# Kernel optimization log

Measured on AMD Instinct MI355X. Metric: run time of the kernel, lower is better.

The kernel has to match this reference:

```python
import jax, jax.numpy as jnp
import numpy as np

N_NODES = 100000
N_EDGES = 1600000
D = 128


def _gine_layer(x, src, dst, e, W1, b1, W2, b2):
    # message: relu(x_j + e_ji), aggregate: sum at destination
    m = jax.nn.relu(x[src] + e)                       # [E, D]
    agg = jax.ops.segment_sum(m, dst, num_segments=x.shape[0])  # [N, D]
    h = agg + x                                       # (1 + eps) * x_i with eps = 0
    h = jax.nn.relu(jnp.dot(h, W1) + b1)
    return jnp.dot(h, W2) + b2


def setup_inputs() -> dict:
    key = jax.random.key(0)
    ks = jax.random.split(key, 16)
    s = 0.05
    inp = {
        "x": jax.random.normal(ks[0], (N_NODES, D), dtype=jnp.float32),
        "edge_index": jax.random.randint(ks[1], (2, N_EDGES), 0, N_NODES, dtype=jnp.int64) if jax.config.jax_enable_x64 else jax.random.randint(ks[1], (2, N_EDGES), 0, N_NODES, dtype=jnp.int32),
        "edge_attr": jax.random.randint(ks[2], (N_EDGES,), 0, 100, dtype=jnp.int32),
        "edge_emb": jax.random.normal(ks[3], (100, D), dtype=jnp.float32) * s,
        "Win": jax.random.normal(ks[4], (D, D), dtype=jnp.float32) * s,
        "b_in": jnp.zeros((D,), dtype=jnp.float32),
        "W1_0": jax.random.normal(ks[5], (D, D), dtype=jnp.float32) * s,
        "b1_0": jnp.zeros((D,), dtype=jnp.float32),
        "W2_0": jax.random.normal(ks[6], (D, D), dtype=jnp.float32) * s,
        "b2_0": jnp.zeros((D,), dtype=jnp.float32),
        "W1_1": jax.random.normal(ks[7], (D, D), dtype=jnp.float32) * s,
        "b1_1": jnp.zeros((D,), dtype=jnp.float32),
        "W2_1": jax.random.normal(ks[8], (D, D), dtype=jnp.float32) * s,
        "b2_1": jnp.zeros((D,), dtype=jnp.float32),
        "Wout": jax.random.normal(ks[9], (D, 1), dtype=jnp.float32) * s,
        "b_out": jnp.zeros((1,), dtype=jnp.float32),
    }
    return inp


def reference(x, edge_index, edge_attr, edge_emb, Win, b_in,
              W1_0, b1_0, W2_0, b2_0, W1_1, b1_1, W2_1, b2_1,
              Wout, b_out):
    src, dst = edge_index[0], edge_index[1]
    e = edge_emb[edge_attr]                 # [E, D] edge-attribute embedding lookup
    h = jnp.dot(x, Win) + b_in              # input_proj
    # layer 0: GINEConv + residual add + relu (norm=none, dropout off)
    h = jax.nn.relu(_gine_layer(h, src, dst, e, W1_0, b1_0, W2_0, b2_0) + h)
    # layer 1
    h = jax.nn.relu(_gine_layer(h, src, dst, e, W1_1, b1_1, W2_1, b2_1) + h)
    # output_mlp: single Linear(hidden, 1); no final activation, no pooling
    return jnp.dot(h, Wout) + b_out
```

## Files before the change

kernel.cpp:

```cpp
#include <hip/hip_runtime.h>

#define NN 100000
#define D 128
#define CHUNK 4096
#define BCSTRIDE 392
#define AGG_BLOCKS 1024

typedef __attribute__((ext_vector_type(8))) short short8;
typedef __attribute__((ext_vector_type(8))) unsigned short ushort8;
typedef __attribute__((ext_vector_type(4))) float f32x4;

__device__ __forceinline__ float4 ld4(const float* p) { return *(const float4*)p; }

__device__ __forceinline__ unsigned short f2bf(float f) {
    unsigned int u = __float_as_uint(f);
    unsigned int r = u + 0x7fffu + ((u >> 16) & 1u);
    return (unsigned short)(r >> 16);
}
__device__ __forceinline__ float bf2f(unsigned short h) {
    return __uint_as_float(((unsigned int)h) << 16);
}
__device__ __forceinline__ int swz(int r, int c) {
    return r * 128 + ((((c >> 2) ^ (r & 7)) << 2) | (c & 3));
}

__device__ __forceinline__ void coop_gemm(
    const unsigned int* uT,
    const unsigned short* __restrict__ Whi, const unsigned short* __restrict__ Wlo,
    int wv, int L, int lr, int q, f32x4 acc[4][2])
{
    #pragma unroll
    for (int ks = 0; ks < 4; ++ks) {
        short8 ahi[4], alo[4];
        #pragma unroll
        for (int m = 0; m < 4; ++m) {
            const int row = m * 16 + lr;
            const int cb  = ks * 32 + q * 8;
            const uint4 a0 = *(const uint4*)&uT[swz(row, cb)];
            const uint4 a1 = *(const uint4*)&uT[swz(row, cb + 4)];
            const unsigned int w[8] = {a0.x, a0.y, a0.z, a0.w, a1.x, a1.y, a1.z, a1.w};
            #pragma unroll
            for (int j = 0; j < 8; ++j) {
                ahi[m][j] = (short)(w[j] >> 16);
                alo[m][j] = (short)(w[j] & 0xffffu);
            }
        }
        #pragma unroll
        for (int n = 0; n < 2; ++n) {
            const int nt = wv * 2 + n;
            const int base = ((nt * 4 + ks) * 64 + L) * 8;
            const short8 bhi = *(const short8*)&Whi[base];
            const short8 blo = *(const short8*)&Wlo[base];
            #pragma unroll
            for (int m = 0; m < 4; ++m) {
                acc[m][n] = __builtin_amdgcn_mfma_f32_16x16x32_bf16(alo[m], bhi, acc[m][n], 0, 0, 0);
                acc[m][n] = __builtin_amdgcn_mfma_f32_16x16x32_bf16(ahi[m], blo, acc[m][n], 0, 0, 0);
                acc[m][n] = __builtin_amdgcn_mfma_f32_16x16x32_bf16(ahi[m], bhi, acc[m][n], 0, 0, 0);
            }
        }
    }
}

__device__ __forceinline__ void gemm_in_body(
    unsigned int* uT, int bid,
    const float* __restrict__ A1,
    const unsigned short* __restrict__ Whi, const unsigned short* __restrict__ Wlo,
    const float* __restrict__ bias,
    unsigned short* __restrict__ out_hi, unsigned short* __restrict__ out_lo, int N)
{
    const int t  = threadIdx.x;
    const int wv = t >> 6;
    const int L  = t & 63;
    const int lr = L & 15;
    const int q  = L >> 4;
    const int rbase = wv * 16;
    const int row = bid * 64 + rbase + lr;
    const int rl  = rbase + lr;

    #pragma unroll
    for (int ks = 0; ks < 4; ++ks) {
        float v[8];
        if (row < N) {
            const int off = row * D + ks * 32 + q * 8;
            const float4 x0 = ld4(&A1[off]), x1 = ld4(&A1[off + 4]);
            v[0] = x0.x; v[1] = x0.y; v[2] = x0.z; v[3] = x0.w;
            v[4] = x1.x; v[5] = x1.y; v[6] = x1.z; v[7] = x1.w;
        } else {
            #pragma unroll
            for (int j = 0; j < 8; ++j) v[j] = 0.f;
        }
        unsigned int pk[8];
        #pragma unroll
        for (int j = 0; j < 8; ++j) {
            const unsigned int hi = f2bf(v[j]);
            pk[j] = (hi << 16) | f2bf(v[j] - bf2f((unsigned short)hi));
        }
        const int cb = ks * 32 + q * 8;
        *(uint4*)&uT[swz(rl, cb)]     = make_uint4(pk[0], pk[1], pk[2], pk[3]);
        *(uint4*)&uT[swz(rl, cb + 4)] = make_uint4(pk[4], pk[5], pk[6], pk[7]);
    }
    __syncthreads();

    f32x4 acc[4][2];
    #pragma unroll
    for (int m = 0; m < 4; ++m)
        #pragma unroll
        for (int n = 0; n < 2; ++n) acc[m][n] = (f32x4){0.f, 0.f, 0.f, 0.f};
    coop_gemm(uT, Whi, Wlo, wv, L, lr, q, acc);
    __syncthreads();

    #pragma unroll
    for (int n = 0; n < 2; ++n) {
        const int nt = wv * 2 + n;
        const float b = bias[nt * 16 + lr];
        #pragma unroll
        for (int m = 0; m < 4; ++m)
            #pragma unroll
            for (int r = 0; r < 4; ++r)
                uT[swz(m * 16 + q * 4 + r, nt * 16 + lr)] = __float_as_uint(acc[m][n][r] + b);
    }
    __syncthreads();

    if (row < N) {
        #pragma unroll
        for (int ks = 0; ks < 4; ++ks) {
            const int cb = ks * 32 + q * 8;
            const uint4 a0 = *(const uint4*)&uT[swz(rl, cb)];
            const uint4 a1 = *(const uint4*)&uT[swz(rl, cb + 4)];
            const unsigned int w[8] = {a0.x, a0.y, a0.z, a0.w, a1.x, a1.y, a1.z, a1.w};
            const int off = row * D + cb;
            ushort8 oh, ol;
            #pragma unroll
            for (int j = 0; j < 8; ++j) {
                const float o = __uint_as_float(w[j]);
                const unsigned short h = f2bf(o);
                oh[j] = h;
                ol[j] = f2bf(o - bf2f(h));
            }
            *(ushort8*)&out_hi[off] = oh;
            *(ushort8*)&out_lo[off] = ol;
        }
    }
}

__global__ __launch_bounds__(256) void setup_all(
    const float* __restrict__ W0, const float* __restrict__ W1,
    const float* __restrict__ W2, const float* __restrict__ W3,
    const float* __restrict__ W4, unsigned short* __restrict__ wp,
    const float* __restrict__ emb, unsigned int* __restrict__ embp,
    int* __restrict__ binTotal)
{
    const int T = blockIdx.x * 256 + threadIdx.x;
    if (T < 5 * D * D) {
        const int w = T / (D * D);
        const int t = T % (D * D);
        const float* W = (w == 0) ? W0 : (w == 1) ? W1 : (w == 2) ? W2 : (w == 3) ? W3 : W4;
        const int j  = t & 7;
        const int L  = (t >> 3) & 63;
        const int ks = (t >> 9) & 3;
        const int nt = t >> 11;
        const float v = W[(ks * 32 + (L >> 4) * 8 + j) * D + nt * 16 + (L & 15)];
        const unsigned short h = f2bf(v);
        unsigned short* hi = wp + (size_t)w * 2 * D * D;
        hi[t] = h;
        hi[D * D + t] = f2bf(v - bf2f(h));
    } else if (T < 5 * D * D + 6400) {
        const int i = T - 5 * D * D;
        embp[i] = (unsigned int)f2bf(emb[i * 2]) | ((unsigned int)f2bf(emb[i * 2 + 1]) << 16);
    } else if (T < 5 * D * D + 6400 + BCSTRIDE) {
        binTotal[T - 5 * D * D - 6400] = 0;
    }
}

__global__ __launch_bounds__(256) void fuse_count_gemm(
    const int* __restrict__ dst, int* __restrict__ blkcnt,
    int* __restrict__ binTotal, int E, int nbins, int csrB,
    const float* __restrict__ A1,
    const unsigned short* __restrict__ Whi, const unsigned short* __restrict__ Wlo,
    const float* __restrict__ bias,
    unsigned short* __restrict__ out_hi, unsigned short* __restrict__ out_lo,
    int N, int gemmBase)
{
    __shared__ __align__(16) unsigned int uT[64 * 128];
    if ((int)blockIdx.x < csrB) {
        int* hist = (int*)uT;
        const int t = threadIdx.x;
        const int i = blockIdx.x;
        for (int k = t; k < nbins; k += 256) hist[k] = 0;
        __syncthreads();
        const int e0 = i * CHUNK;
        const int e1 = min(E, e0 + CHUNK);
        for (int e = e0 + t; e < e1; e += 256) atomicAdd(&hist[dst[e] >> 8], 1);
        __syncthreads();
        for (int k = t; k < nbins; k += 256) {
            const int c = hist[k];
            blkcnt[i * BCSTRIDE + k] = c;
            if (c) atomicAdd(&binTotal[k], c);
        }
    } else {
        gemm_in_body(uT, blockIdx.x - csrB + gemmBase, A1, Whi, Wlo, bias, out_hi, out_lo, N);
    }
}

__global__ __launch_bounds__(512) void bin_scan(
    const int* __restrict__ binTotal, int* __restrict__ binStart,
    int* __restrict__ binCursor, int nbins)
{
    __shared__ int s[512];
    const int t = threadIdx.x;
    const int v = (t < nbins) ? binTotal[t] : 0;
    s[t] = v;
    __syncthreads();
    for (int off = 1; off < 512; off <<= 1) {
        const int x = (t >= off) ? s[t - off] : 0;
        __syncthreads();
        s[t] += x;
        __syncthreads();
    }
    if (t < nbins) { binStart[t] = s[t] - v; binCursor[t] = s[t] - v; }
    if (t == 0)    binStart[nbins] = s[511];
}

__global__ __launch_bounds__(256) void fuse_scatter_gemm(
    const int* __restrict__ src, const int* __restrict__ dst,
    const int* __restrict__ attr, const int* __restrict__ blkcnt,
    int* __restrict__ binCursor, int2* __restrict__ binned, int E, int nbins, int csrB,
    const float* __restrict__ A1,
    const unsigned short* __restrict__ Whi, const unsigned short* __restrict__ Wlo,
    const float* __restrict__ bias,
    unsigned short* __restrict__ out_hi, unsigned short* __restrict__ out_lo,
    int N, int gemmBase)
{
    __shared__ __align__(16) unsigned int uT[64 * 128];
    if ((int)blockIdx.x < csrB) {
        int* cur = (int*)uT;
        const int t = threadIdx.x;
        const int i = blockIdx.x;
        for (int k = t; k < nbins; k += 256) {
            const int c = blkcnt[i * BCSTRIDE + k];
            if (c) cur[k] = atomicAdd(&binCursor[k], c);
        }
        __syncthreads();
        const int e0 = i * CHUNK;
        const int e1 = min(E, e0 + CHUNK);
        for (int e = e0 + t; e < e1; e += 256) {
            const int d = dst[e];
            const int p = atomicAdd(&cur[d >> 8], 1);
            binned[p] = make_int2(src[e] | (attr[e] << 20), d);
        }
    } else {
        gemm_in_body(uT, blockIdx.x - csrB + gemmBase, A1, Whi, Wlo, bias, out_hi, out_lo, N);
    }
}

__global__ __launch_bounds__(256) void fuse_build_gemm(
    const int2* __restrict__ binned, const int* __restrict__ binStart,
    int* __restrict__ rowptr, int* __restrict__ epack, int csrB,
    const float* __restrict__ A1,
    const unsigned short* __restrict__ Whi, const unsigned short* __restrict__ Wlo,
    const float* __restrict__ bias,
    unsigned short* __restrict__ out_hi, unsigned short* __restrict__ out_lo,
    int N, int gemmBase)
{
    __shared__ __align__(16) unsigned int uT[64 * 128];
    if ((int)blockIdx.x < csrB) {
        int* hist = (int*)uT;
        int* scn  = (int*)uT + 256;
        int* curn = (int*)uT + 512;
        const int t = threadIdx.x;
        const int b = blockIdx.x;
        hist[t] = 0;
        __syncthreads();
        const int ebeg = binStart[b];
        const int eend = binStart[b + 1];
        for (int e = ebeg + t; e < eend; e += 256) atomicAdd(&hist[binned[e].y & 255], 1);
        __syncthreads();
        scn[t] = hist[t];
        __syncthreads();
        for (int off = 1; off < 256; off <<= 1) {
            const int x = (t >= off) ? scn[t - off] : 0;
            __syncthreads();
            scn[t] += x;
            __syncthreads();
        }
        const int node = b * 256 + t;
        if (node < N) rowptr[node] = ebeg + scn[t];
        curn[t] = ebeg + scn[t] - hist[t];
        __syncthreads();
        for (int e = ebeg + t; e < eend; e += 256) {
            const int2 v = binned[e];
            const int p = atomicAdd(&curn[v.y & 255], 1);
            epack[p] = v.x;
        }
    } else {
        gemm_in_body(uT, blockIdx.x - csrB + gemmBase, A1, Whi, Wlo, bias, out_hi, out_lo, N);
    }
}

template<bool LAST>
__global__ __launch_bounds__(256) void mlp_fused(
    const float* __restrict__ agg,
    const unsigned short* h_hi, const unsigned short* h_lo,
    const unsigned short* __restrict__ W1hi, const unsigned short* __restrict__ W1lo,
    const float* __restrict__ b1,
    const unsigned short* __restrict__ W2hi, const unsigned short* __restrict__ W2lo,
    const float* __restrict__ b2,
    unsigned short* out_hi, unsigned short* out_lo,
    const float* __restrict__ Wout, const float* __restrict__ bout,
    float* __restrict__ outv, int N)
{
    __shared__ __align__(16) unsigned int uT[64 * 128];
    const int t  = threadIdx.x;
    const int wv = t >> 6;
    const int L  = t & 63;
    const int lr = L & 15;
    const int q  = L >> 4;
    const int rbase = wv * 16;
    const int row = blockIdx.x * 64 + rbase + lr;
    const int rl  = rbase + lr;

    #pragma unroll
    for (int ks = 0; ks < 4; ++ks) {
        float v[8];
        if (row < N) {
            const int off = row * D + ks * 32 + q * 8;
            const float4 x0 = ld4(&agg[off]), x1 = ld4(&agg[off + 4]);
            const ushort8 hh = *(const ushort8*)&h_hi[off];
            const ushort8 ll = *(const ushort8*)&h_lo[off];
            v[0] = x0.x; v[1] = x0.y; v[2] = x0.z; v[3] = x0.w;
            v[4] = x1.x; v[5] = x1.y; v[6] = x1.z; v[7] = x1.w;
            #pragma unroll
            for (int j = 0; j < 8; ++j) v[j] += bf2f(hh[j]) + bf2f(ll[j]);
        } else {
            #pragma unroll
            for (int j = 0; j < 8; ++j) v[j] = 0.f;
        }
        unsigned int pk[8];
        #pragma unroll
        for (int j = 0; j < 8; ++j) {
            const unsigned int hi = f2bf(v[j]);
            pk[j] = (hi << 16) | f2bf(v[j] - bf2f((unsigned short)hi));
        }
        const int cb = ks * 32 + q * 8;
        *(uint4*)&uT[swz(rl, cb)]     = make_uint4(pk[0], pk[1], pk[2], pk[3]);
        *(uint4*)&uT[swz(rl, cb + 4)] = make_uint4(pk[4], pk[5], pk[6], pk[7]);
    }
    __syncthreads();

    f32x4 acc[4][2];
    #pragma unroll
    for (int m = 0; m < 4; ++m)
        #pragma unroll
        for (int n = 0; n < 2; ++n) acc[m][n] = (f32x4){0.f, 0.f, 0.f, 0.f};
    coop_gemm(uT, W1hi, W1lo, wv, L, lr, q, acc);
    __syncthreads();

    #pragma unroll
    for (int n = 0; n < 2; ++n) {
        const int nt = wv * 2 + n;
        const float b = b1[nt * 16 + lr];
        #pragma unroll
        for (int m = 0; m < 4; ++m)
            #pragma unroll
            for (int r = 0; r < 4; ++r) {
                const float o = fmaxf(acc[m][n][r] + b, 0.f);
                const unsigned int hi = f2bf(o);
                const unsigned int lo = f2bf(o - bf2f((unsigned short)hi));
                uT[swz(m * 16 + q * 4 + r, nt * 16 + lr)] = (hi << 16) | lo;
            }
    }
    __syncthreads();

    f32x4 acc2[4][2];
    #pragma unroll
    for (int m = 0; m < 4; ++m)
        #pragma unroll
        for (int n = 0; n < 2; ++n) acc2[m][n] = (f32x4){0.f, 0.f, 0.f, 0.f};
    coop_gemm(uT, W2hi, W2lo, wv, L, lr, q, acc2);
    __syncthreads();

    #pragma unroll
    for (int n = 0; n < 2; ++n) {
        const int nt = wv * 2 + n;
        const float b = b2[nt * 16 + lr];
        #pragma unroll
        for (int m = 0; m < 4; ++m)
            #pragma unroll
            for (int r = 0; r < 4; ++r)
                uT[swz(m * 16 + q * 4 + r, nt * 16 + lr)] = __float_as_uint(acc2[m][n][r] + b);
    }
    __syncthreads();

    if (LAST) {
        float accv = 0.f;
        if (row < N) {
            #pragma unroll
            for (int ks = 0; ks < 4; ++ks) {
                const int cb = ks * 32 + q * 8;
                const uint4 a0 = *(const uint4*)&uT[swz(rl, cb)];
                const uint4 a1 = *(const uint4*)&uT[swz(rl, cb + 4)];
                const unsigned int w[8] = {a0.x, a0.y, a0.z, a0.w, a1.x, a1.y, a1.z, a1.w};
                const int off = row * D + cb;
                const ushort8 hh = *(const ushort8*)&h_hi[off];
                const ushort8 ll = *(const ushort8*)&h_lo[off];
                const float4 w0 = ld4(&Wout[cb]);
                const float4 w1 = ld4(&Wout[cb + 4]);
                float o[8];
                #pragma unroll
                for (int j = 0; j < 8; ++j)
                    o[j] = fmaxf(__uint_as_float(w[j]) + bf2f(hh[j]) + bf2f(ll[j]), 0.f);
                accv += o[0] * w0.x + o[1] * w0.y + o[2] * w0.z + o[3] * w0.w;
                accv += o[4] * w1.x + o[5] * w1.y + o[6] * w1.z + o[7] * w1.w;
            }
        }
        accv += __shfl_xor(accv, 16);
        accv += __shfl_xor(accv, 32);
        if (q == 0 && row < N) outv[row] = accv + bout[0];
    } else if (row < N) {
        #pragma unroll
        for (int ks = 0; ks < 4; ++ks) {
            const int cb = ks * 32 + q * 8;
            const uint4 a0 = *(const uint4*)&uT[swz(rl, cb)];
            const uint4 a1 = *(const uint4*)&uT[swz(rl, cb + 4)];
            const unsigned int w[8] = {a0.x, a0.y, a0.z, a0.w, a1.x, a1.y, a1.z, a1.w};
            const int off = row * D + cb;
            const ushort8 hh = *(const ushort8*)&h_hi[off];
            const ushort8 ll = *(const ushort8*)&h_lo[off];
            ushort8 oh, ol;
            #pragma unroll
            for (int j = 0; j < 8; ++j) {
                const float o = fmaxf(__uint_as_float(w[j]) + bf2f(hh[j]) + bf2f(ll[j]), 0.f);
                const unsigned short h = f2bf(o);
                oh[j] = h;
                ol[j] = f2bf(o - bf2f(h));
            }
            *(ushort8*)&out_hi[off] = oh;
            *(ushort8*)&out_lo[off] = ol;
        }
    }
}

__global__ __launch_bounds__(512) void aggregate(
    const unsigned int* __restrict__ hu,
    const int* __restrict__ rowptr, const int* __restrict__ epack,
    const unsigned int* __restrict__ embp, float* __restrict__ agg, int N)
{
    __shared__ unsigned int semb[100 * 64];
    const int t = threadIdx.x;
    for (int i = t; i < 100 * 64; i += 512) semb[i] = embp[i];
    __syncthreads();

    const int wv   = t >> 6;
    const int lane = t & 63;

    for (int node = blockIdx.x * 8 + wv; node < N; node += AGG_BLOCKS * 8) {
        int start = (node == 0) ? 0 : rowptr[node - 1];
        int end   = rowptr[node];
        start = __builtin_amdgcn_readfirstlane(start);
        end   = __builtin_amdgcn_readfirstlane(end);

        float ax = 0.f, ay = 0.f;
        int j = start;

        for (; j < end && (j & 3); ++j) {
            const int p0 = __builtin_amdgcn_readfirstlane(epack[j]);
            const unsigned int u0 = hu[(p0 & 0xFFFFF) * 64 + lane];
            const unsigned int v0 = semb[(p0 >> 20) * 64 + lane];
            ax += fmaxf(__uint_as_float(u0 << 16) + __uint_as_float(v0 << 16), 0.f);
            ay += fmaxf(__uint_as_float(u0 & 0xffff0000u) + __uint_as_float(v0 & 0xffff0000u), 0.f);
        }

        for (; j + 7 < end; j += 8) {
            const int4 pk0 = *(const int4*)&epack[j];
            const int4 pk1 = *(const int4*)&epack[j + 4];
            int p[8];
            p[0] = __builtin_amdgcn_readfirstlane(pk0.x);
            p[1] = __builtin_amdgcn_readfirstlane(pk0.y);
            p[2] = __builtin_amdgcn_readfirstlane(pk0.z);
            p[3] = __builtin_amdgcn_readfirstlane(pk0.w);
            p[4] = __builtin_amdgcn_readfirstlane(pk1.x);
            p[5] = __builtin_amdgcn_readfirstlane(pk1.y);
            p[6] = __builtin_amdgcn_readfirstlane(pk1.z);
            p[7] = __builtin_amdgcn_readfirstlane(pk1.w);
            unsigned int u[8], v[8];
            #pragma unroll
            for (int k = 0; k < 8; ++k) u[k] = hu[(p[k] & 0xFFFFF) * 64 + lane];
            #pragma unroll
            for (int k = 0; k < 8; ++k) v[k] = semb[(p[k] >> 20) * 64 + lane];
            #pragma unroll
            for (int k = 0; k < 8; ++k) {
                ax += fmaxf(__uint_as_float(u[k] << 16) + __uint_as_float(v[k] << 16), 0.f);
                ay += fmaxf(__uint_as_float(u[k] & 0xffff0000u) + __uint_as_float(v[k] & 0xffff0000u), 0.f);
            }
        }

        if (j + 3 < end) {
            const int4 pk0 = *(const int4*)&epack[j];
            int p[4];
            p[0] = __builtin_amdgcn_readfirstlane(pk0.x);
            p[1] = __builtin_amdgcn_readfirstlane(pk0.y);
            p[2] = __builtin_amdgcn_readfirstlane(pk0.z);
            p[3] = __builtin_amdgcn_readfirstlane(pk0.w);
            unsigned int u[4], v[4];
            #pragma unroll
            for (int k = 0; k < 4; ++k) u[k] = hu[(p[k] & 0xFFFFF) * 64 + lane];
            #pragma unroll
            for (int k = 0; k < 4; ++k) v[k] = semb[(p[k] >> 20) * 64 + lane];
            #pragma unroll
            for (int k = 0; k < 4; ++k) {
                ax += fmaxf(__uint_as_float(u[k] << 16) + __uint_as_float(v[k] << 16), 0.f);
                ay += fmaxf(__uint_as_float(u[k] & 0xffff0000u) + __uint_as_float(v[k] & 0xffff0000u), 0.f);
            }
            j += 4;
        }

        for (; j < end; ++j) {
            const int p0 = __builtin_amdgcn_readfirstlane(epack[j]);
            const unsigned int u0 = hu[(p0 & 0xFFFFF) * 64 + lane];
            const unsigned int v0 = semb[(p0 >> 20) * 64 + lane];
            ax += fmaxf(__uint_as_float(u0 << 16) + __uint_as_float(v0 << 16), 0.f);
            ay += fmaxf(__uint_as_float(u0 & 0xffff0000u) + __uint_as_float(v0 & 0xffff0000u), 0.f);
        }

        float2 o; o.x = ax; o.y = ay;
        ((float2*)agg)[node * 64 + lane] = o;
    }
}

extern "C" void kernel_launch(void* const* d_in, const int* in_sizes, int n_in,
                              void* d_out, int out_size, void* d_ws, size_t ws_size,
                              hipStream_t stream)
{
    const float* x     = (const float*)d_in[0];
    const int*   ei    = (const int*)  d_in[1];
    const int*   attr  = (const int*)  d_in[2];
    const float* emb   = (const float*)d_in[3];
    const float* Win   = (const float*)d_in[4];
    const float* b_in  = (const float*)d_in[5];
    const float* W1_0  = (const float*)d_in[6];
    const float* b1_0  = (const float*)d_in[7];
    const float* W2_0  = (const float*)d_in[8];
    const float* b2_0  = (const float*)d_in[9];
    const float* W1_1  = (const float*)d_in[10];
    const float* b1_1  = (const float*)d_in[11];
    const float* W2_1  = (const float*)d_in[12];
    const float* b2_1  = (const float*)d_in[13];
    const float* Wout  = (const float*)d_in[14];
    const float* b_out = (const float*)d_in[15];
    float* out = (float*)d_out;

    const int N = NN;
    const int E = in_sizes[2];
    const int* srcp = ei;
    const int* dstp = ei + E;
    const int nbins = (N + 255) >> 8;
    const int eblocks = (E + CHUNK - 1) / CHUNK;

    unsigned short* h_hi = (unsigned short*)d_ws;
    unsigned short* h_lo = h_hi + (size_t)N * D;
    float* agg    = (float*)(h_lo + (size_t)N * D);
    int*   rowptr = (int*)(agg + (size_t)N * D);
    int*   epack  = rowptr + N;
    unsigned short* wp = (unsigned short*)(epack + E);
    unsigned short* Whi[5], *Wlo[5];
    for (int i = 0; i < 5; ++i) {
        Whi[i] = wp + (size_t)i * 2 * D * D;
        Wlo[i] = Whi[i] + D * D;
    }
    unsigned int* embp = (unsigned int*)(wp + 5 * 2 * D * D);
    int2* binned    = (int2*)agg;
    int*  blkcnt    = (int*)(binned + E);
    int*  binTotal  = blkcnt + eblocks * BCSTRIDE;
    int*  binStart  = binTotal + BCSTRIDE;
    int*  binCursor = binStart + BCSTRIDE;

    dim3 blk(256);
    const int fgrid = (N + 63) / 64;
    const int sgrid = (5 * D * D + 6400 + BCSTRIDE + 255) / 256;

    const int G1 = 200;
    const int G2 = 700;
    const int G3 = fgrid - G1 - G2;

    setup_all<<<sgrid, blk, 0, stream>>>(Win, W1_0, W2_0, W1_1, W2_1, wp, emb, embp, binTotal);

    fuse_count_gemm<<<eblocks + G1, blk, 0, stream>>>(
        dstp, blkcnt, binTotal, E, nbins, eblocks,
        x, Whi[0], Wlo[0], b_in, h_hi, h_lo, N, 0);
    bin_scan<<<1, 512, 0, stream>>>(binTotal, binStart, binCursor, nbins);
    fuse_scatter_gemm<<<eblocks + G2, blk, 0, stream>>>(
        srcp, dstp, attr, blkcnt, binCursor, binned, E, nbins, eblocks,
        x, Whi[0], Wlo[0], b_in, h_hi, h_lo, N, G1);
    fuse_build_gemm<<<nbins + G3, blk, 0, stream>>>(
        binned, binStart, rowptr, epack, nbins,
        x, Whi[0], Wlo[0], b_in, h_hi, h_lo, N, G1 + G2);

    aggregate<<<AGG_BLOCKS, dim3(512), 0, stream>>>(
        (const unsigned int*)h_hi, rowptr, epack, embp, agg, N);
    mlp_fused<false><<<fgrid, blk, 0, stream>>>(
        agg, h_hi, h_lo, Whi[1], Wlo[1], b1_0, Whi[2], Wlo[2], b2_0,
        h_hi, h_lo, nullptr, nullptr, nullptr, N);

    aggregate<<<AGG_BLOCKS, dim3(512), 0, stream>>>(
        (const unsigned int*)h_hi, rowptr, epack, embp, agg, N);
    mlp_fused<true><<<fgrid, blk, 0, stream>>>(
        agg, h_hi, h_lo, Whi[3], Wlo[3], b1_1, Whi[4], Wlo[4], b2_1,
        nullptr, nullptr, Wout, b_out, out, N);
}
```

Baseline: 429.6 us.

## Use 8-wave 512-thread blocks for fused GEMM and CSR-build kernels

Doubles the block size of the fused GEMM, CSR count/scatter/build and MLP kernels from 256 to 512 threads. Each wave now owns one 16-column output tile instead of two. The global load/store mapping is reorganised so each lane handles 16 contiguous columns of one row, with the final output reduction done over 8 lanes. The aim is more waves in flight per 64-row tile and fewer B-operand loads per wave, at the cost of more threads contending for the same shared-memory tile and barriers, and larger per-thread register arrays.

```diff
diff --git a/kernel.cpp b/kernel.cpp
--- a/kernel.cpp
+++ b/kernel.cpp
@@ -24,10 +24,10 @@
     return r * 128 + ((((c >> 2) ^ (r & 7)) << 2) | (c & 3));
 }
 
-__device__ __forceinline__ void coop_gemm(
+__device__ __forceinline__ void coop_gemm8(
     const unsigned int* uT,
     const unsigned short* __restrict__ Whi, const unsigned short* __restrict__ Wlo,
-    int wv, int L, int lr, int q, f32x4 acc[4][2])
+    int wv, int lane, int lr, int q, f32x4 acc[4])
 {
     #pragma unroll
     for (int ks = 0; ks < 4; ++ks) {
@@ -45,18 +45,14 @@
                 alo[m][j] = (short)(w[j] & 0xffffu);
             }
         }
-        #pragma unroll
-        for (int n = 0; n < 2; ++n) {
-            const int nt = wv * 2 + n;
-            const int base = ((nt * 4 + ks) * 64 + L) * 8;
-            const short8 bhi = *(const short8*)&Whi[base];
-            const short8 blo = *(const short8*)&Wlo[base];
-            #pragma unroll
-            for (int m = 0; m < 4; ++m) {
-                acc[m][n] = __builtin_amdgcn_mfma_f32_16x16x32_bf16(alo[m], bhi, acc[m][n], 0, 0, 0);
-                acc[m][n] = __builtin_amdgcn_mfma_f32_16x16x32_bf16(ahi[m], blo, acc[m][n], 0, 0, 0);
-                acc[m][n] = __builtin_amdgcn_mfma_f32_16x16x32_bf16(ahi[m], bhi, acc[m][n], 0, 0, 0);
-            }
+        const int base = ((wv * 4 + ks) * 64 + lane) * 8;
+        const short8 bhi = *(const short8*)&Whi[base];
+        const short8 blo = *(const short8*)&Wlo[base];
+        #pragma unroll
+        for (int m = 0; m < 4; ++m) {
+            acc[m] = __builtin_amdgcn_mfma_f32_16x16x32_bf16(alo[m], bhi, acc[m], 0, 0, 0);
+            acc[m] = __builtin_amdgcn_mfma_f32_16x16x32_bf16(ahi[m], blo, acc[m], 0, 0, 0);
+            acc[m] = __builtin_amdgcn_mfma_f32_16x16x32_bf16(ahi[m], bhi, acc[m], 0, 0, 0);
         }
     }
 }
@@ -68,77 +64,78 @@
     const float* __restrict__ bias,
     unsigned short* __restrict__ out_hi, unsigned short* __restrict__ out_lo, int N)
 {
-    const int t  = threadIdx.x;
-    const int wv = t >> 6;
-    const int L  = t & 63;
-    const int lr = L & 15;
-    const int q  = L >> 4;
-    const int rbase = wv * 16;
-    const int row = bid * 64 + rbase + lr;
-    const int rl  = rbase + lr;
-
+    const int t    = threadIdx.x;
+    const int wv   = t >> 6;
+    const int lane = t & 63;
+    const int lr   = lane & 15;
+    const int q    = lane >> 4;
+    const int rE   = wv * 8 + (lane >> 3);
+    const int cE   = (lane & 7) * 16;
+    const int rowE = bid * 64 + rE;
+
+    {
+        float v[16];
+        if (rowE < N) {
+            const int off = rowE * D + cE;
+            #pragma unroll
+            for (int k = 0; k < 4; ++k) {
+                const float4 x = ld4(&A1[off + k * 4]);
+                v[k * 4 + 0] = x.x; v[k * 4 + 1] = x.y; v[k * 4 + 2] = x.z; v[k * 4 + 3] = x.w;
+            }
+        } else {
+            #pragma unroll
+            for (int j = 0; j < 16; ++j) v[j] = 0.f;
+        }
+        #pragma unroll
+        for (int k = 0; k < 4; ++k) {
+            unsigned int pk[4];
+            #pragma unroll
+            for (int j = 0; j < 4; ++j) {
+                const float f = v[k * 4 + j];
+                const unsigned int hi = f2bf(f);
+                pk[j] = (hi << 16) | f2bf(f - bf2f((unsigned short)hi));
+            }
+            *(uint4*)&uT[swz(rE, cE + k * 4)] = make_uint4(pk[0], pk[1], pk[2], pk[3]);
+        }
+    }
+    __syncthreads();
+
+    f32x4 acc[4];
     #pragma unroll
-    for (int ks = 0; ks < 4; ++ks) {
-        float v[8];
-        if (row < N) {
-            const int off = row * D + ks * 32 + q * 8;
-            const float4 x0 = ld4(&A1[off]), x1 = ld4(&A1[off + 4]);
-            v[0] = x0.x; v[1] = x0.y; v[2] = x0.z; v[3] = x0.w;
-            v[4] = x1.x; v[5] = x1.y; v[6] = x1.z; v[7] = x1.w;
-        } else {
-            #pragma unroll
-            for (int j = 0; j < 8; ++j) v[j] = 0.f;
-        }
-        unsigned int pk[8];
-        #pragma unroll
-        for (int j = 0; j < 8; ++j) {
-            const unsigned int hi = f2bf(v[j]);
-            pk[j] = (hi << 16) | f2bf(v[j] - bf2f((unsigned short)hi));
-        }
-        const int cb = ks * 32 + q * 8;
-        *(uint4*)&uT[swz(rl, cb)]     = make_uint4(pk[0], pk[1], pk[2], pk[3]);
-        *(uint4*)&uT[swz(rl, cb + 4)] = make_uint4(pk[4], pk[5], pk[6], pk[7]);
-    }
-    __syncthreads();
-
-    f32x4 acc[4][2];
-    #pragma unroll
-    for (int m = 0; m < 4; ++m)
-        #pragma unroll
-        for (int n = 0; n < 2; ++n) acc[m][n] = (f32x4){0.f, 0.f, 0.f, 0.f};
-    coop_gemm(uT, Whi, Wlo, wv, L, lr, q, acc);
-    __syncthreads();
-
-    #pragma unroll
-    for (int n = 0; n < 2; ++n) {
-        const int nt = wv * 2 + n;
-        const float b = bias[nt * 16 + lr];
+    for (int m = 0; m < 4; ++m) acc[m] = (f32x4){0.f, 0.f, 0.f, 0.f};
+    coop_gemm8(uT, Whi, Wlo, wv, lane, lr, q, acc);
+    __syncthreads();
+
+    {
+        const float b = bias[wv * 16 + lr];
         #pragma unroll
         for (int m = 0; m < 4; ++m)
             #pragma unroll
             for (int r = 0; r < 4; ++r)
-                uT[swz(m * 16 + q * 4 + r, nt * 16 + lr)] = __float_as_uint(acc[m][n][r] + b);
-    }
-    __syncthreads();
-
-    if (row < N) {
-        #pragma unroll
-        for (int ks = 0; ks < 4; ++ks) {
-            const int cb = ks * 32 + q * 8;
-            const uint4 a0 = *(const uint4*)&uT[swz(rl, cb)];
-            const uint4 a1 = *(const uint4*)&uT[swz(rl, cb + 4)];
-            const unsigned int w[8] = {a0.x, a0.y, a0.z, a0.w, a1.x, a1.y, a1.z, a1.w};
-            const int off = row * D + cb;
+                uT[swz(m * 16 + q * 4 + r, wv * 16 + lr)] = __float_as_uint(acc[m][r] + b);
+    }
+    __syncthreads();
+
+    if (rowE < N) {
+        const int off = rowE * D + cE;
+        unsigned int w[16];
+        #pragma unroll
+        for (int k = 0; k < 4; ++k) {
+            const uint4 a = *(const uint4*)&uT[swz(rE, cE + k * 4)];
+            w[k * 4 + 0] = a.x; w[k * 4 + 1] = a.y; w[k * 4 + 2] = a.z; w[k * 4 + 3] = a.w;
+        }
+        #pragma unroll
+        for (int h8 = 0; h8 < 2; ++h8) {
             ushort8 oh, ol;
             #pragma unroll
             for (int j = 0; j < 8; ++j) {
-                const float o = __uint_as_float(w[j]);
+                const float o = __uint_as_float(w[h8 * 8 + j]);
                 const unsigned short h = f2bf(o);
                 oh[j] = h;
                 ol[j] = f2bf(o - bf2f(h));
             }
-            *(ushort8*)&out_hi[off] = oh;
-            *(ushort8*)&out_lo[off] = ol;
+            *(ushort8*)&out_hi[off + h8 * 8] = oh;
+            *(ushort8*)&out_lo[off + h8 * 8] = ol;
         }
     }
 }
@@ -172,7 +169,7 @@
     }
 }
 
-__global__ __launch_bounds__(256) void fuse_count_gemm(
+__global__ __launch_bounds__(512, 8) void fuse_count_gemm(
     const int* __restrict__ dst, int* __restrict__ blkcnt,
     int* __restrict__ binTotal, int E, int nbins, int csrB,
     const float* __restrict__ A1,
@@ -186,13 +183,13 @@
         int* hist = (int*)uT;
         const int t = threadIdx.x;
         const int i = blockIdx.x;
-        for (int k = t; k < nbins; k += 256) hist[k] = 0;
+        for (int k = t; k < nbins; k += 512) hist[k] = 0;
         __syncthreads();
         const int e0 = i * CHUNK;
         const int e1 = min(E, e0 + CHUNK);
-        for (int e = e0 + t; e < e1; e += 256) atomicAdd(&hist[dst[e] >> 8], 1);
-        __syncthreads();
-        for (int k = t; k < nbins; k += 256) {
+        for (int e = e0 + t; e < e1; e += 512) atomicAdd(&hist[dst[e] >> 8], 1);
+        __syncthreads();
+        for (int k = t; k < nbins; k += 512) {
             const int c = hist[k];
             blkcnt[i * BCSTRIDE + k] = c;
             if (c) atomicAdd(&binTotal[k], c);
@@ -221,7 +218,7 @@
     if (t == 0)    binStart[nbins] = s[511];
 }
 
-__global__ __launch_bounds__(256) void fuse_scatter_gemm(
+__global__ __launch_bounds__(512, 8) void fuse_scatter_gemm(
     const int* __restrict__ src, const int* __restrict__ dst,
     const int* __restrict__ attr, const int* __restrict__ blkcnt,
     int* __restrict__ binCursor, int2* __restrict__ binned, int E, int nbins, int csrB,
@@ -236,14 +233,14 @@
         int* cur = (int*)uT;
         const int t = threadIdx.x;
         const int i = blockIdx.x;
-        for (int k = t; k < nbins; k += 256) {
+        for (int k = t; k < nbins; k += 512) {
             const int c = blkcnt[i * BCSTRIDE + k];
             if (c) cur[k] = atomicAdd(&binCursor[k], c);
         }
         __syncthreads();
         const int e0 = i * CHUNK;
         const int e1 = min(E, e0 + CHUNK);
-        for (int e = e0 + t; e < e1; e += 256) {
+        for (int e = e0 + t; e < e1; e += 512) {
             const int d = dst[e];
             const int p = atomicAdd(&cur[d >> 8], 1);
             binned[p] = make_int2(src[e] | (attr[e] << 20), d);
@@ -253,7 +250,7 @@
     }
 }
 
-__global__ __launch_bounds__(256) void fuse_build_gemm(
+__global__ __launch_bounds__(512, 8) void fuse_build_gemm(
     const int2* __restrict__ binned, const int* __restrict__ binStart,
     int* __restrict__ rowptr, int* __restrict__ epack, int csrB,
     const float* __restrict__ A1,
@@ -269,25 +266,28 @@
         int* curn = (int*)uT + 512;
         const int t = threadIdx.x;
         const int b = blockIdx.x;
-        hist[t] = 0;
+        if (t < 256) hist[t] = 0;
         __syncthreads();
         const int ebeg = binStart[b];
         const int eend = binStart[b + 1];
-        for (int e = ebeg + t; e < eend; e += 256) atomicAdd(&hist[binned[e].y & 255], 1);
-        __syncthreads();
-        scn[t] = hist[t];
+        for (int e = ebeg + t; e < eend; e += 512) atomicAdd(&hist[binned[e].y & 255], 1);
+        __syncthreads();
+        if (t < 256) scn[t] = hist[t];
         __syncthreads();
         for (int off = 1; off < 256; off <<= 1) {
-            const int x = (t >= off) ? scn[t - off] : 0;
+            int x = 0;
+            if (t < 256 && t >= off) x = scn[t - off];
             __syncthreads();
-            scn[t] += x;
+            if (t < 256) scn[t] += x;
             __syncthreads();
         }
-        const int node = b * 256 + t;
-        if (node < N) rowptr[node] = ebeg + scn[t];
-        curn[t] = ebeg + scn[t] - hist[t];
-        __syncthreads();
-        for (int e = ebeg + t; e < eend; e += 256) {
+        if (t < 256) {
+            const int node = b * 256 + t;
+            if (node < N) rowptr[node] = ebeg + scn[t];
+            curn[t] = ebeg + scn[t] - hist[t];
+        }
+        __syncthreads();
+        for (int e = ebeg + t; e < eend; e += 512) {
             const int2 v = binned[e];
             const int p = atomicAdd(&curn[v.y & 255], 1);
             epack[p] = v.x;
@@ -298,7 +298,7 @@
 }
 
 template<bool LAST>
-__global__ __launch_bounds__(256) void mlp_fused(
+__global__ __launch_bounds__(512, 8) void mlp_fused(
     const float* __restrict__ agg,
     const unsigned short* h_hi, const unsigned short* h_lo,
     const unsigned short* __restrict__ W1hi, const unsigned short* __restrict__ W1lo,
@@ -310,132 +310,135 @@
     float* __restrict__ outv, int N)
 {
     __shared__ __align__(16) unsigned int uT[64 * 128];
-    const int t  = threadIdx.x;
-    const int wv = t >> 6;
-    const int L  = t & 63;
-    const int lr = L & 15;
-    const int q  = L >> 4;
-    const int rbase = wv * 16;
-    const int row = blockIdx.x * 64 + rbase + lr;
-    const int rl  = rbase + lr;
-
+    const int t    = threadIdx.x;
+    const int wv   = t >> 6;
+    const int lane = t & 63;
+    const int lr   = lane & 15;
+    const int q    = lane >> 4;
+    const int rE   = wv * 8 + (lane >> 3);
+    const int cE   = (lane & 7) * 16;
+    const int rowE = blockIdx.x * 64 + rE;
+
+    {
+        float v[16];
+        if (rowE < N) {
+            const int off = rowE * D + cE;
+            #pragma unroll
+            for (int k = 0; k < 4; ++k) {
+                const float4 x = ld4(&agg[off + k * 4]);
+                v[k * 4 + 0] = x.x; v[k * 4 + 1] = x.y; v[k * 4 + 2] = x.z; v[k * 4 + 3] = x.w;
+            }
+            #pragma unroll
+            for (int h8 = 0; h8 < 2; ++h8) {
+                const ushort8 hh = *(const ushort8*)&h_hi[off + h8 * 8];
+                const ushort8 ll = *(const ushort8*)&h_lo[off + h8 * 8];
+                #pragma unroll
+                for (int j = 0; j < 8; ++j) v[h8 * 8 + j] += bf2f(hh[j]) + bf2f(ll[j]);
+            }
+        } else {
+            #pragma unroll
+            for (int j = 0; j < 16; ++j) v[j] = 0.f;
+        }
+        #pragma unroll
+        for (int k = 0; k < 4; ++k) {
+            unsigned int pk[4];
+            #pragma unroll
+            for (int j = 0; j < 4; ++j) {
+                const float f = v[k * 4 + j];
+                const unsigned int hi = f2bf(f);
+                pk[j] = (hi << 16) | f2bf(f - bf2f((unsigned short)hi));
+            }
+            *(uint4*)&uT[swz(rE, cE + k * 4)] = make_uint4(pk[0], pk[1], pk[2], pk[3]);
+        }
+    }
+    __syncthreads();
+
+    f32x4 acc[4];
     #pragma unroll
-    for (int ks = 0; ks < 4; ++ks) {
-        float v[8];
-        if (row < N) {
-            const int off = row * D + ks * 32 + q * 8;
-            const float4 x0 = ld4(&agg[off]), x1 = ld4(&agg[off + 4]);
-            const ushort8 hh = *(const ushort8*)&h_hi[off];
-            const ushort8 ll = *(const ushort8*)&h_lo[off];
-            v[0] = x0.x; v[1] = x0.y; v[2] = x0.z; v[3] = x0.w;
-            v[4] = x1.x; v[5] = x1.y; v[6] = x1.z; v[7] = x1.w;
-            #pragma unroll
-            for (int j = 0; j < 8; ++j) v[j] += bf2f(hh[j]) + bf2f(ll[j]);
-        } else {
-            #pragma unroll
-            for (int j = 0; j < 8; ++j) v[j] = 0.f;
-        }
-        unsigned int pk[8];
-        #pragma unroll
-        for (int j = 0; j < 8; ++j) {
-            const unsigned int hi = f2bf(v[j]);
-            pk[j] = (hi << 16) | f2bf(v[j] - bf2f((unsigned short)hi));
-        }
-        const int cb = ks * 32 + q * 8;
-        *(uint4*)&uT[swz(rl, cb)]     = make_uint4(pk[0], pk[1], pk[2], pk[3]);
-        *(uint4*)&uT[swz(rl, cb + 4)] = make_uint4(pk[4], pk[5], pk[6], pk[7]);
-    }
-    __syncthreads();
-
-    f32x4 acc[4][2];
-    #pragma unroll
-    for (int m = 0; m < 4; ++m)
-        #pragma unroll
-        for (int n = 0; n < 2; ++n) acc[m][n] = (f32x4){0.f, 0.f, 0.f, 0.f};
-    coop_gemm(uT, W1hi, W1lo, wv, L, lr, q, acc);
-    __syncthreads();
-
-    #pragma unroll
-    for (int n = 0; n < 2; ++n) {
-        const int nt = wv * 2 + n;
-        const float b = b1[nt * 16 + lr];
+    for (int m = 0; m < 4; ++m) acc[m] = (f32x4){0.f, 0.f, 0.f, 0.f};
+    coop_gemm8(uT, W1hi, W1lo, wv, lane, lr, q, acc);
+    __syncthreads();
+
+    {
+        const float b = b1[wv * 16 + lr];
         #pragma unroll
         for (int m = 0; m < 4; ++m)
             #pragma unroll
             for (int r = 0; r < 4; ++r) {
-                const float o = fmaxf(acc[m][n][r] + b, 0.f);
+                const float o = fmaxf(acc[m][r] + b, 0.f);
                 const unsigned int hi = f2bf(o);
                 const unsigned int lo = f2bf(o - bf2f((unsigned short)hi));
-                uT[swz(m * 16 + q * 4 + r, nt * 16 + lr)] = (hi << 16) | lo;
-            }
-    }
-    __syncthreads();
-
-    f32x4 acc2[4][2];
+                uT[swz(m * 16 + q * 4 + r, wv * 16 + lr)] = (hi << 16) | lo;
+            }
+    }
+    __syncthreads();
+
+    f32x4 acc2[4];
     #pragma unroll
-    for (int m = 0; m < 4; ++m)
-        #pragma unroll
-        for (int n = 0; n < 2; ++n) acc2[m][n] = (f32x4){0.f, 0.f, 0.f, 0.f};
-    coop_gemm(uT, W2hi, W2lo, wv, L, lr, q, acc2);
-    __syncthreads();
-
-    #pragma unroll
-    for (int n = 0; n < 2; ++n) {
-        const int nt = wv * 2 + n;
-        const float b = b2[nt * 16 + lr];
+    for (int m = 0; m < 4; ++m) acc2[m] = (f32x4){0.f, 0.f, 0.f, 0.f};
+    coop_gemm8(uT, W2hi, W2lo, wv, lane, lr, q, acc2);
+    __syncthreads();
+
+    {
+        const float b = b2[wv * 16 + lr];
         #pragma unroll
         for (int m = 0; m < 4; ++m)
             #pragma unroll
             for (int r = 0; r < 4; ++r)
-                uT[swz(m * 16 + q * 4 + r, nt * 16 + lr)] = __float_as_uint(acc2[m][n][r] + b);
+                uT[swz(m * 16 + q * 4 + r, wv * 16 + lr)] = __float_as_uint(acc2[m][r] + b);
     }
     __syncthreads();
 
     if (LAST) {
         float accv = 0.f;
-        if (row < N) {
-            #pragma unroll
-            for (int ks = 0; ks < 4; ++ks) {
-                const int cb = ks * 32 + q * 8;
-                const uint4 a0 = *(const uint4*)&uT[swz(rl, cb)];
-                const uint4 a1 = *(const uint4*)&uT[swz(rl, cb + 4)];
-                const unsigned int w[8] = {a0.x, a0.y, a0.z, a0.w, a1.x, a1.y, a1.z, a1.w};
-                const int off = row * D + cb;
-                const ushort8 hh = *(const ushort8*)&h_hi[off];
-                const ushort8 ll = *(const ushort8*)&h_lo[off];
-                const float4 w0 = ld4(&Wout[cb]);
-                const float4 w1 = ld4(&Wout[cb + 4]);
+        if (rowE < N) {
+            const int off = rowE * D + cE;
+            unsigned int w[16];
+            #pragma unroll
+            for (int k = 0; k < 4; ++k) {
+                const uint4 a = *(const uint4*)&uT[swz(rE, cE + k * 4)];
+                w[k * 4 + 0] = a.x; w[k * 4 + 1] = a.y; w[k * 4 + 2] = a.z; w[k * 4 + 3] = a.w;
+            }
+            #pragma unroll
+            for (int h8 = 0; h8 < 2; ++h8) {
+                const ushort8 hh = *(const ushort8*)&h_hi[off + h8 * 8];
+                const ushort8 ll = *(const ushort8*)&h_lo[off + h8 * 8];
+                const float4 w0 = ld4(&Wout[cE + h8 * 8]);
+                const float4 w1 = ld4(&Wout[cE + h8 * 8 + 4]);
                 float o[8];
                 #pragma unroll
                 for (int j = 0; j < 8; ++j)
-                    o[j] = fmaxf(__uint_as_float(w[j]) + bf2f(hh[j]) + bf2f(ll[j]), 0.f);
+                    o[j] = fmaxf(__uint_as_float(w[h8 * 8 + j]) + bf2f(hh[j]) + bf2f(ll[j]), 0.f);
                 accv += o[0] * w0.x + o[1] * w0.y + o[2] * w0.z + o[3] * w0.w;
                 accv += o[4] * w1.x + o[5] * w1.y + o[6] * w1.z + o[7] * w1.w;
             }
         }
-        accv += __shfl_xor(accv, 16);
-        accv += __shfl_xor(accv, 32);
-        if (q == 0 && row < N) outv[row] = accv + bout[0];
-    } else if (row < N) {
-        #pragma unroll
-        for (int ks = 0; ks < 4; ++ks) {
-            const int cb = ks * 32 + q * 8;
-            const uint4 a0 = *(const uint4*)&uT[swz(rl, cb)];
-            const uint4 a1 = *(const uint4*)&uT[swz(rl, cb + 4)];
-            const unsigned int w[8] = {a0.x, a0.y, a0.z, a0.w, a1.x, a1.y, a1.z, a1.w};
-            const int off = row * D + cb;
-            const ushort8 hh = *(const ushort8*)&h_hi[off];
-            const ushort8 ll = *(const ushort8*)&h_lo[off];
+        accv += __shfl_xor(accv, 1);
+        accv += __shfl_xor(accv, 2);
+        accv += __shfl_xor(accv, 4);
+        if ((lane & 7) == 0 && rowE < N) outv[rowE] = accv + bout[0];
+    } else if (rowE < N) {
+        const int off = rowE * D + cE;
+        unsigned int w[16];
+        #pragma unroll
+        for (int k = 0; k < 4; ++k) {
+            const uint4 a = *(const uint4*)&uT[swz(rE, cE + k * 4)];
+            w[k * 4 + 0] = a.x; w[k * 4 + 1] = a.y; w[k * 4 + 2] = a.z; w[k * 4 + 3] = a.w;
+        }
+        #pragma unroll
+        for (int h8 = 0; h8 < 2; ++h8) {
+            const ushort8 hh = *(const ushort8*)&h_hi[off + h8 * 8];
+            const ushort8 ll = *(const ushort8*)&h_lo[off + h8 * 8];
             ushort8 oh, ol;
             #pragma unroll
             for (int j = 0; j < 8; ++j) {
-                const float o = fmaxf(__uint_as_float(w[j]) + bf2f(hh[j]) + bf2f(ll[j]), 0.f);
+                const float o = fmaxf(__uint_as_float(w[h8 * 8 + j]) + bf2f(hh[j]) + bf2f(ll[j]), 0.f);
                 const unsigned short h = f2bf(o);
                 oh[j] = h;
                 ol[j] = f2bf(o - bf2f(h));
             }
-            *(ushort8*)&out_hi[off] = oh;
-            *(ushort8*)&out_lo[off] = ol;
+            *(ushort8*)&out_hi[off + h8 * 8] = oh;
+            *(ushort8*)&out_lo[off + h8 * 8] = ol;
         }
     }
 }
@@ -574,7 +577,6 @@
     int*  binStart  = binTotal + BCSTRIDE;
     int*  binCursor = binStart + BCSTRIDE;
 
-    dim3 blk(256);
     const int fgrid = (N + 63) / 64;
     const int sgrid = (5 * D * D + 6400 + BCSTRIDE + 255) / 256;
 
@@ -582,28 +584,28 @@
     const int G2 = 700;
     const int G3 = fgrid - G1 - G2;
 
-    setup_all<<<sgrid, blk, 0, stream>>>(Win, W1_0, W2_0, W1_1, W2_1, wp, emb, embp, binTotal);
-
-    fuse_count_gemm<<<eblocks + G1, blk, 0, stream>>>(
+    setup_all<<<sgrid, dim3(256), 0, stream>>>(Win, W1_0, W2_0, W1_1, W2_1, wp, emb, embp, binTotal);
+
+    fuse_count_gemm<<<eblocks + G1, dim3(512), 0, stream>>>(
         dstp, blkcnt, binTotal, E, nbins, eblocks,
         x, Whi[0], Wlo[0], b_in, h_hi, h_lo, N, 0);
     bin_scan<<<1, 512, 0, stream>>>(binTotal, binStart, binCursor, nbins);
-    fuse_scatter_gemm<<<eblocks + G2, blk, 0, stream>>>(
+    fuse_scatter_gemm<<<eblocks + G2, dim3(512), 0, stream>>>(
         srcp, dstp, attr, blkcnt, binCursor, binned, E, nbins, eblocks,
         x, Whi[0], Wlo[0], b_in, h_hi, h_lo, N, G1);
-    fuse_build_gemm<<<nbins + G3, blk, 0, stream>>>(
+    fuse_build_gemm<<<nbins + G3, dim3(512), 0, stream>>>(
         binned, binStart, rowptr, epack, nbins,
         x, Whi[0], Wlo[0], b_in, h_hi, h_lo, N, G1 + G2);
 
     aggregate<<<AGG_BLOCKS, dim3(512), 0, stream>>>(
         (const unsigned int*)h_hi, rowptr, epack, embp, agg, N);
-    mlp_fused<false><<<fgrid, blk, 0, stream>>>(
+    mlp_fused<false><<<fgrid, dim3(512), 0, stream>>>(
         agg, h_hi, h_lo, Whi[1], Wlo[1], b1_0, Whi[2], Wlo[2], b2_0,
         h_hi, h_lo, nullptr, nullptr, nullptr, N);
 
     aggregate<<<AGG_BLOCKS, dim3(512), 0, stream>>>(
         (const unsigned int*)h_hi, rowptr, epack, embp, agg, N);
-    mlp_fused<true><<<fgrid, blk, 0, stream>>>(
+    mlp_fused<true><<<fgrid, dim3(512), 0, stream>>>(
         agg, h_hi, h_lo, Whi[3], Wlo[3], b1_1, Whi[4], Wlo[4], b2_1,
         nullptr, nullptr, Wout, b_out, out, N);
 }
```

Measured after the change: 418.9 us. -2.5%, faster.
